# Kernel optimization log

Hardware: AMD Instinct MI355X
Metric: run time of the kernel (lower is better)

Reference implementation:

```python
import jax, jax.numpy as jnp
import numpy as np

D_MODEL = 1024
N_HEAD = 16
HEAD_DIM = D_MODEL // N_HEAD
D_FF = int(D_MODEL * 4.0)
B, T = 2, 2048


def rms_norm(x, eps=1e-6):
    return x * jax.lax.rsqrt(jnp.mean(jnp.square(x), axis=-1, keepdims=True) + eps)


def rope_tables(T, head_dim):
    # half-truncated RoPE: first quarter of dims get real freqs, next quarter zeros
    angular_freq = (1.0 / 1024.0) ** jnp.linspace(0.0, 1.0, head_dim // 4, dtype=jnp.float32)
    angular_freq = jnp.concatenate([angular_freq, jnp.zeros(head_dim // 4, jnp.float32)])
    theta = jnp.arange(T, dtype=jnp.float32)[:, None] * angular_freq[None, :]  # [T, head_dim//2]
    return jnp.cos(theta), jnp.sin(theta)


def apply_rope(x, cos, sin):
    # x: [B, H, T, D]; cos/sin: [T, D//2]
    x1, x2 = jnp.split(x.astype(jnp.float32), 2, axis=-1)
    c = cos[None, None]
    s = sin[None, None]
    y1 = x1 * c + x2 * s
    y2 = -x1 * s + x2 * c
    return jnp.concatenate([y1, y2], axis=-1).astype(x.dtype)


def setup_inputs() -> dict:
    key = jax.random.key(0)
    ks = jax.random.split(key, 10)
    x = jax.random.normal(ks[0], (B, T, D_MODEL), jnp.float32)
    block_mask = jnp.tril(jnp.ones((T, T), jnp.bool_))  # causal
    sc = 1.0 / np.sqrt(D_MODEL)
    Wqkv = jax.random.normal(ks[1], (D_MODEL, 3 * D_MODEL), jnp.float32) * sc
    bqkv = jnp.zeros((3 * D_MODEL,), jnp.float32)
    Wo = jax.random.normal(ks[2], (D_MODEL, D_MODEL), jnp.float32) * sc
    bo = jnp.zeros((D_MODEL,), jnp.float32)
    W1 = jax.random.normal(ks[3], (D_MODEL, D_FF), jnp.float32) * sc
    b1 = jnp.zeros((D_FF,), jnp.float32)
    W2 = jax.random.normal(ks[4], (D_FF, D_MODEL), jnp.float32) * (1.0 / np.sqrt(D_FF))
    b2 = jnp.zeros((D_MODEL,), jnp.float32)
    return {"x": x, "block_mask": block_mask, "Wqkv": Wqkv, "bqkv": bqkv,
            "Wo": Wo, "bo": bo, "W1": W1, "b1": b1, "W2": W2, "b2": b2}


def reference(x, block_mask, Wqkv, bqkv, Wo, bo, W1, b1, W2, b2):
    Bq, Tq, D = x.shape
    cos, sin = rope_tables(Tq, HEAD_DIM)

    def attn(h):
        qkv = h @ Wqkv + bqkv  # [B, T, 3D]
        qkv = qkv.reshape(Bq, Tq, 3, N_HEAD, HEAD_DIM)
        qkv = jnp.transpose(qkv, (2, 0, 3, 1, 4))  # [3, B, H, T, d]
        q, k, v = qkv[0], qkv[1], qkv[2]
        q, k = rms_norm(q), rms_norm(k)
        q, k = apply_rope(q, cos, sin), apply_rope(k, cos, sin)
        scores = jnp.einsum('bhtd,bhsd->bhts', q, k) / np.sqrt(HEAD_DIM)
        scores = jnp.where(block_mask[None, None], scores, jnp.float32(-1e30))
        p = jax.nn.softmax(scores, axis=-1)
        o = jnp.einsum('bhts,bhsd->bhtd', p, v)
        o = jnp.transpose(o, (0, 2, 1, 3)).reshape(Bq, Tq, D)
        return o @ Wo + bo

    def mlp(h):
        return jax.nn.gelu(h @ W1 + b1) @ W2 + b2

    x = x + attn(rms_norm(x))
    x = x + mlp(rms_norm(x))
    return x
```

## Files before the change

### kernel.cpp

```cpp
#include <hip/hip_runtime.h>
#include <hip/hip_bf16.h>


typedef __attribute__((ext_vector_type(8))) short short8;
typedef __attribute__((ext_vector_type(4))) float f32x4;
typedef __attribute__((ext_vector_type(8))) unsigned short u16x8;

#define MROWS 4096
#define DMODEL 1024
#define DFF 4096
#define NH 16
#define HD 64
#define SEQ 2048

static __device__ __forceinline__ unsigned short f2bf(float f) {
    union { __hip_bfloat16 b; unsigned short u; } cv;
    cv.b = __float2bfloat16(f);
    return cv.u;
}

static __device__ __forceinline__ void gload_lds16(const void* g, void* l) {
    __builtin_amdgcn_global_load_lds(
        (const __attribute__((address_space(1))) unsigned int*)g,
        (__attribute__((address_space(3))) unsigned int*)l, 16, 0, 0);
}

static __device__ __forceinline__ int xcd_swizzle(int id, int nwg) {
    const int nx = 8;
    const int q = nwg / nx, r = nwg % nx;
    const int xcd = id % nx, loc = id / nx;
    return (xcd < r ? xcd * (q + 1) : r * (q + 1) + (xcd - r) * q) + loc;
}

__global__ void cast_transpose(const float* __restrict__ W,
                               unsigned short* __restrict__ Wt, int K, int N) {
    __shared__ float tile[32][33];
    const int tx = threadIdx.x & 31;
    const int ty = threadIdx.x >> 5;
    const int n0 = blockIdx.x * 32, k0 = blockIdx.y * 32;
#pragma unroll
    for (int i = 0; i < 4; ++i) {
        int kk = ty + i * 8;
        tile[kk][tx] = W[(long)(k0 + kk) * N + n0 + tx];
    }
    __syncthreads();
#pragma unroll
    for (int i = 0; i < 4; ++i) {
        int nn = ty + i * 8;
        Wt[(long)(n0 + nn) * K + k0 + tx] = f2bf(tile[tx][nn]);
    }
}

__global__ void rope_table(float* __restrict__ cosT, float* __restrict__ sinT) {
    const int t = blockIdx.x, j = threadIdx.x;
    float th = (j < 16) ? (float)t * exp2f(-(10.0f / 15.0f) * (float)j) : 0.0f;
    cosT[t * 32 + j] = cosf(th);
    sinT[t * 32 + j] = sinf(th);
}

__global__ void rmsnorm_cast(const float* __restrict__ xin,
                             unsigned short* __restrict__ hout) {
    const int row = blockIdx.x;
    const float4 v = ((const float4*)(xin + (long)row * DMODEL))[threadIdx.x];
    float ss = v.x * v.x + v.y * v.y + v.z * v.z + v.w * v.w;
#pragma unroll
    for (int m = 32; m >= 1; m >>= 1) ss += __shfl_xor(ss, m);
    __shared__ float part[4];
    if ((threadIdx.x & 63) == 0) part[threadIdx.x >> 6] = ss;
    __syncthreads();
    const float tot = part[0] + part[1] + part[2] + part[3];
    const float sc = rsqrtf(tot * (1.0f / (float)DMODEL) + 1e-6f);
    ushort4 o;
    o.x = f2bf(v.x * sc); o.y = f2bf(v.y * sc);
    o.z = f2bf(v.z * sc); o.w = f2bf(v.w * sc);
    ((ushort4*)hout)[(long)row * (DMODEL / 4) + threadIdx.x] = o;
}

template <int EPI, int BN>
__launch_bounds__(256)
__global__ void gemm_bt(const short* __restrict__ A, const short* __restrict__ Bt,
                        const float* __restrict__ bias, const float* __restrict__ res,
                        float* __restrict__ outF, unsigned short* __restrict__ outB,
                        int N, int K) {
    constexpr int NF = BN / 32;
    __shared__ short As[2][128 * 32];
    __shared__ short Bs[2][BN * 32];
    const int tid = threadIdx.x;
    const int lane = tid & 63, w = tid >> 6;
    const int wr = w >> 1, wc = w & 1;
    const int l16 = lane & 15, lhi = lane >> 4;

    const int nwg = gridDim.x * gridDim.y;
    int id = xcd_swizzle(blockIdx.y * gridDim.x + blockIdx.x, nwg);
    const int bx = id % gridDim.x, by = id / gridDim.x;
    const long rowA0 = (long)by * 128;
    const long rowB0 = (long)bx * BN;

    const f32x4 fz = {0.f, 0.f, 0.f, 0.f};
    f32x4 acc[4][NF];
#pragma unroll
    for (int m = 0; m < 4; ++m)
#pragma unroll
        for (int n = 0; n < NF; ++n) acc[m][n] = fz;

    auto stage = [&](int kt, int b) {
        const int k0 = kt << 5;
#pragma unroll
        for (int it = 0; it < 2; ++it) {
            const int c = it * 256 + tid;
            const int r = c >> 2, col = (c & 3) << 3;
            gload_lds16(A + (rowA0 + r) * K + k0 + col, (char*)As[b] + c * 16);
        }
#pragma unroll
        for (int it = 0; it < BN / 64; ++it) {
            const int c = it * 256 + tid;
            const int r = c >> 2, col = (c & 3) << 3;
            gload_lds16(Bt + (rowB0 + r) * K + k0 + col, (char*)Bs[b] + c * 16);
        }
    };
    auto compute = [&](int b) {
        short8 af[4], bf[NF];
#pragma unroll
        for (int m = 0; m < 4; ++m)
            af[m] = *(const short8*)(&As[b][0] + (wr * 64 + m * 16 + l16) * 32 + lhi * 8);
#pragma unroll
        for (int n = 0; n < NF; ++n)
            bf[n] = *(const short8*)(&Bs[b][0] + (wc * (BN / 2) + n * 16 + l16) * 32 + lhi * 8);
#pragma unroll
        for (int m = 0; m < 4; ++m)
#pragma unroll
            for (int n = 0; n < NF; ++n)
                acc[m][n] = __builtin_amdgcn_mfma_f32_16x16x32_bf16(
                    af[m], bf[n], acc[m][n], 0, 0, 0);
    };

    const int ktiles = K >> 5;
    stage(0, 0);
    __syncthreads();
    int cur = 0;
    for (int kt = 0; kt < ktiles; ++kt) {
        if (kt + 1 < ktiles) stage(kt + 1, cur ^ 1);
        compute(cur);
        __syncthreads();
        cur ^= 1;
    }

#pragma unroll
    for (int m = 0; m < 4; ++m) {
        const long r0 = rowA0 + wr * 64 + m * 16 + lhi * 4;
#pragma unroll
        for (int n = 0; n < NF; ++n) {
            const long cc = rowB0 + wc * (BN / 2) + n * 16 + l16;
            const float bv = bias[cc];
#pragma unroll
            for (int j = 0; j < 4; ++j) {
                const long idx = (r0 + j) * N + cc;
                float v = acc[m][n][j] + bv;
                if (EPI == 1) v += res[idx];
                if (EPI == 2) {
                    float g = 0.5f * v *
                        (1.0f + tanhf(0.7978845608028654f * (v + 0.044715f * v * v * v)));
                    outB[idx] = f2bf(g);
                } else {
                    outF[idx] = v;
                }
            }
        }
    }
}

__global__ void qkv_post(const float* __restrict__ qkv, const float* __restrict__ cosT,
                         const float* __restrict__ sinT, unsigned short* __restrict__ Qo,
                         unsigned short* __restrict__ Ko) {
    const int lane = threadIdx.x & 63;
    const int g = blockIdx.x * 4 + (threadIdx.x >> 6);
    const int row = g >> 4, h = g & 15;
    const int b = row >> 11, t = row & 2047;
    const float* base = qkv + (long)row * 3072 + h * 64;
    float q = base[lane];
    float k = base[1024 + lane];
    float sq = q * q, sk = k * k;
#pragma unroll
    for (int m = 32; m >= 1; m >>= 1) {
        sq += __shfl_xor(sq, m);
        sk += __shfl_xor(sk, m);
    }
    q *= rsqrtf(sq * (1.0f / 64.0f) + 1e-6f);
    k *= rsqrtf(sk * (1.0f / 64.0f) + 1e-6f);
    const int j = lane & 31;
    const float c = cosT[t * 32 + j], s = sinT[t * 32 + j];
    const float q2 = __shfl_xor(q, 32), k2 = __shfl_xor(k, 32);
    const float sgn = (lane < 32) ? 1.0f : -1.0f;
    const float qr = q * c + sgn * q2 * s;
    const float kr = k * c + sgn * k2 * s;
    const long o = ((long)(b * 16 + h) * SEQ + t) * 64 + lane;
    Qo[o] = f2bf(qr * 0.125f);
    Ko[o] = f2bf(kr);
}

__global__ void transpose_v(const float* __restrict__ qkv,
                            unsigned short* __restrict__ Vt) {
    __shared__ float tile[64][65];
    const int tid = threadIdx.x;
    const int bh = blockIdx.x, tt = blockIdx.y;
    const int b = bh >> 4, h = bh & 15;
    const int tr = tid >> 2, c0 = (tid & 3) * 16;
    const float* src = qkv + ((long)(b * SEQ + tt * 64 + tr)) * 3072 + 2048 + h * 64 + c0;
#pragma unroll
    for (int i = 0; i < 4; ++i) {
        float4 v = ((const float4*)src)[i];
        tile[tr][c0 + i * 4 + 0] = v.x;
        tile[tr][c0 + i * 4 + 1] = v.y;
        tile[tr][c0 + i * 4 + 2] = v.z;
        tile[tr][c0 + i * 4 + 3] = v.w;
    }
    __syncthreads();
    const int d = tid >> 2, t0 = (tid & 3) * 16;
    unsigned short* dst = Vt + ((long)bh * 64 + d) * SEQ + tt * 64 + t0;
#pragma unroll
    for (int half = 0; half < 2; ++half) {
        u16x8 o;
#pragma unroll
        for (int e = 0; e < 8; ++e) o[e] = f2bf(tile[t0 + half * 8 + e][d]);
        *(u16x8*)(dst + half * 8) = o;
    }
}

__launch_bounds__(256)
__global__ void attn_fwd(const short* __restrict__ Qg, const short* __restrict__ Kg,
                         const short* __restrict__ Vtg, unsigned short* __restrict__ Og) {
    __shared__ short Ks[64 * 64];
    __shared__ short Vs[64 * 64];
    __shared__ char Ps[4][16 * 128];
    const int tid = threadIdx.x, lane = tid & 63, w = tid >> 6;
    const int l16 = lane & 15, lhi = lane >> 4;
    int id = xcd_swizzle(blockIdx.y * gridDim.x + blockIdx.x, 1024);
    const int bh = id >> 5;
    const int qt = 31 - (id & 31);
    const int bb = bh >> 4, hh = bh & 15;
    const long base_q = (long)bh * (SEQ * 64);

    short8 aq0, aq1;
    {
        const short* Qp = Qg + base_q + (long)(qt * 64 + w * 16) * 64;
        aq0 = *(const short8*)(Qp + l16 * 64 + lhi * 8);
        aq1 = *(const short8*)(Qp + l16 * 64 + 32 + lhi * 8);
    }
    float mrow[4] = {-1e30f, -1e30f, -1e30f, -1e30f};
    float lrow[4] = {0.f, 0.f, 0.f, 0.f};
    const f32x4 fz = {0.f, 0.f, 0.f, 0.f};
    f32x4 oacc[4];
#pragma unroll
    for (int n = 0; n < 4; ++n) oacc[n] = fz;

    char* Pw = &Ps[w][0];

    for (int kt = 0; kt <= qt; ++kt) {
        const short* Kp = Kg + base_q + (long)kt * 64 * 64;
        const short* Vp = Vtg + base_q + (long)kt * 64;
#pragma unroll
        for (int it = 0; it < 2; ++it) {
            const int c = it * 256 + w * 64 + lane;
            const int r = c >> 3;
            const int col = ((c & 7) ^ (r & 7)) << 3;
            gload_lds16(Kp + r * 64 + col, (char*)Ks + c * 16);
            gload_lds16(Vp + (long)r * SEQ + col, (char*)Vs + c * 16);
        }
        __syncthreads();

        f32x4 s[4];
        __builtin_amdgcn_s_setprio(1);
#pragma unroll
        for (int n = 0; n < 4; ++n) {
            const int kr = n * 16 + l16;
            short8 bk0 = *(const short8*)(Ks + kr * 64 + ((lhi ^ (kr & 7)) << 3));
            short8 bk1 = *(const short8*)(Ks + kr * 64 + (((lhi + 4) ^ (kr & 7)) << 3));
            f32x4 z = fz;
            z = __builtin_amdgcn_mfma_f32_16x16x32_bf16(aq0, bk0, z, 0, 0, 0);
            s[n] = __builtin_amdgcn_mfma_f32_16x16x32_bf16(aq1, bk1, z, 0, 0, 0);
        }
        __builtin_amdgcn_s_setprio(0);
        if (kt == qt) {
#pragma unroll
            for (int n = 0; n < 4; ++n)
#pragma unroll
                for (int j = 0; j < 4; ++j)
                    if (n * 16 + l16 > w * 16 + lhi * 4 + j) s[n][j] = -1e30f;
        }

#pragma unroll
        for (int j = 0; j < 4; ++j) {
            float pm = fmaxf(fmaxf(s[0][j], s[1][j]), fmaxf(s[2][j], s[3][j]));
            pm = fmaxf(pm, __shfl_xor(pm, 1));
            pm = fmaxf(pm, __shfl_xor(pm, 2));
            pm = fmaxf(pm, __shfl_xor(pm, 4));
            pm = fmaxf(pm, __shfl_xor(pm, 8));
            const float newm = fmaxf(mrow[j], pm);
            const float sc = __expf(mrow[j] - newm);
            float ps = 0.f;
#pragma unroll
            for (int n = 0; n < 4; ++n) {
                float p = __expf(s[n][j] - newm);
                s[n][j] = p;
                ps += p;
            }
            ps += __shfl_xor(ps, 1);
            ps += __shfl_xor(ps, 2);
            ps += __shfl_xor(ps, 4);
            ps += __shfl_xor(ps, 8);
            lrow[j] = lrow[j] * sc + ps;
            mrow[j] = newm;
#pragma unroll
            for (int n = 0; n < 4; ++n) oacc[n][j] *= sc;
        }

#pragma unroll
        for (int n = 0; n < 4; ++n)
#pragma unroll
            for (int j = 0; j < 4; ++j) {
                const int q = lhi * 4 + j, colp = n * 16 + l16;
                *(short*)(Pw + ((q * 128 + colp * 2) ^ ((q & 7) << 4))) =
                    (short)f2bf(s[n][j]);
            }
        __builtin_amdgcn_s_setprio(1);
#pragma unroll
        for (int ks = 0; ks < 2; ++ks) {
            short8 pa = *(const short8*)(Pw + ((l16 * 128 + ks * 64 + lhi * 16) ^ ((l16 & 7) << 4)));
#pragma unroll
            for (int n = 0; n < 4; ++n) {
                const int dr = n * 16 + l16;
                short8 vb = *(const short8*)(Vs + dr * 64 + ((((ks << 2) + lhi) ^ (dr & 7)) << 3));
                oacc[n] = __builtin_amdgcn_mfma_f32_16x16x32_bf16(pa, vb, oacc[n], 0, 0, 0);
            }
        }
        __builtin_amdgcn_s_setprio(0);
        __syncthreads();
    }

#pragma unroll
    for (int n = 0; n < 4; ++n)
#pragma unroll
        for (int j = 0; j < 4; ++j) {
            const int qrow = qt * 64 + w * 16 + lhi * 4 + j;
            const long orow = (long)bb * SEQ + qrow;
            const int col = hh * 64 + n * 16 + l16;
            Og[orow * DMODEL + col] = f2bf(oacc[n][j] / lrow[j]);
        }
}

extern "C" void kernel_launch(void* const* d_in, const int* in_sizes, int n_in,
                              void* d_out, int out_size, void* d_ws, size_t ws_size,
                              hipStream_t stream) {
    const float* x    = (const float*)d_in[0];
    const float* Wqkv = (const float*)d_in[2];
    const float* bqkv = (const float*)d_in[3];
    const float* Wo   = (const float*)d_in[4];
    const float* bo   = (const float*)d_in[5];
    const float* W1   = (const float*)d_in[6];
    const float* b1   = (const float*)d_in[7];
    const float* W2   = (const float*)d_in[8];
    const float* b2   = (const float*)d_in[9];
    float* out = (float*)d_out;

    char* ws = (char*)d_ws;
    auto alloc = [&](size_t b) {
        char* p = ws;
        ws += (b + 255) & ~(size_t)255;
        return p;
    };
    short* WqkvT = (short*)alloc(3072ull * 1024 * 2);
    short* WoT   = (short*)alloc(1024ull * 1024 * 2);
    short* W1T   = (short*)alloc(4096ull * 1024 * 2);
    short* W2T   = (short*)alloc(1024ull * 4096 * 2);
    float* cosT  = (float*)alloc(2048ull * 32 * 4);
    float* sinT  = (float*)alloc(2048ull * 32 * 4);
    short* hbuf  = (short*)alloc((size_t)MROWS * DMODEL * 2);
    short* Qb    = (short*)alloc(32ull * SEQ * 64 * 2);
    short* Kb    = (short*)alloc(32ull * SEQ * 64 * 2);
    short* Vtb   = (short*)alloc(32ull * 64 * SEQ * 2);
    short* Ob    = (short*)alloc((size_t)MROWS * DMODEL * 2);
    float* x1    = (float*)alloc((size_t)MROWS * DMODEL * 4);
    char*  big   = alloc((size_t)MROWS * 3072 * 4);
    float* qkv   = (float*)big;
    unsigned short* act = (unsigned short*)big;

    cast_transpose<<<dim3(96, 32), 256, 0, stream>>>(Wqkv, (unsigned short*)WqkvT, 1024, 3072);
    cast_transpose<<<dim3(32, 32), 256, 0, stream>>>(Wo, (unsigned short*)WoT, 1024, 1024);
    cast_transpose<<<dim3(128, 32), 256, 0, stream>>>(W1, (unsigned short*)W1T, 1024, 4096);
    cast_transpose<<<dim3(32, 128), 256, 0, stream>>>(W2, (unsigned short*)W2T, 4096, 1024);
    rope_table<<<2048, 32, 0, stream>>>(cosT, sinT);
    rmsnorm_cast<<<MROWS, 256, 0, stream>>>(x, (unsigned short*)hbuf);
    gemm_bt<0, 128><<<dim3(24, 32), 256, 0, stream>>>(hbuf, WqkvT, bqkv, nullptr, qkv, nullptr, 3072, 1024);
    qkv_post<<<16384, 256, 0, stream>>>(qkv, cosT, sinT,
                                        (unsigned short*)Qb, (unsigned short*)Kb);
    transpose_v<<<dim3(32, 32), 256, 0, stream>>>(qkv, (unsigned short*)Vtb);
    attn_fwd<<<dim3(32, 32), 256, 0, stream>>>(Qb, Kb, Vtb, (unsigned short*)Ob);
    gemm_bt<1, 64><<<dim3(16, 32), 256, 0, stream>>>(Ob, WoT, bo, x, x1, nullptr, 1024, 1024);
    rmsnorm_cast<<<MROWS, 256, 0, stream>>>(x1, (unsigned short*)hbuf);
    gemm_bt<2, 128><<<dim3(32, 32), 256, 0, stream>>>(hbuf, W1T, b1, nullptr, nullptr, act, 4096, 1024);
    gemm_bt<1, 64><<<dim3(16, 32), 256, 0, stream>>>((const short*)act, W2T, b2, x1, out, nullptr, 1024, 4096);
}
```

Baseline: 447.8 us.

## Double-buffer K/V in attention, pair causal tiles per block, lazy rescale

The attention kernel now double-buffers the K and V tiles in LDS, prefetching the next key tile while the current one is computed, which removes the load-then-sync stall of each iteration. Each block handles two query tiles (qt and 31-qt) to balance causal work, and the launch grid is halved to match. The S MFMA operands are swapped so each lane holds a full query row, which cuts the per-row shuffle reductions and lets P be written as packed 4-element stores. Online-softmax rescaling is skipped when the running max grows by no more than 8, trading a small overflow-safety margin for fewer exp and multiply operations. Doubling LDS for K/V may reduce occupancy.

```diff
diff --git a/kernel.cpp b/kernel.cpp
--- a/kernel.cpp
+++ b/kernel.cpp
@@ -4,6 +4,7 @@
 
 typedef __attribute__((ext_vector_type(8))) short short8;
 typedef __attribute__((ext_vector_type(4))) float f32x4;
+typedef __attribute__((ext_vector_type(4))) unsigned short u16x4;
 typedef __attribute__((ext_vector_type(8))) unsigned short u16x8;
 
 #define MROWS 4096
@@ -229,123 +230,143 @@
 __launch_bounds__(256)
 __global__ void attn_fwd(const short* __restrict__ Qg, const short* __restrict__ Kg,
                          const short* __restrict__ Vtg, unsigned short* __restrict__ Og) {
-    __shared__ short Ks[64 * 64];
-    __shared__ short Vs[64 * 64];
-    __shared__ char Ps[4][16 * 128];
+    __shared__ short Ks[2][64 * 64];
+    __shared__ short Vs[2][64 * 64];
+    __shared__ char Ps[4][2048];
     const int tid = threadIdx.x, lane = tid & 63, w = tid >> 6;
     const int l16 = lane & 15, lhi = lane >> 4;
-    int id = xcd_swizzle(blockIdx.y * gridDim.x + blockIdx.x, 1024);
-    const int bh = id >> 5;
-    const int qt = 31 - (id & 31);
+    const int id = xcd_swizzle(blockIdx.y * gridDim.x + blockIdx.x, 512);
+    const int bh = id >> 4;
+    const int ip = id & 15;
     const int bb = bh >> 4, hh = bh & 15;
     const long base_q = (long)bh * (SEQ * 64);
-
-    short8 aq0, aq1;
-    {
-        const short* Qp = Qg + base_q + (long)(qt * 64 + w * 16) * 64;
-        aq0 = *(const short8*)(Qp + l16 * 64 + lhi * 8);
-        aq1 = *(const short8*)(Qp + l16 * 64 + 32 + lhi * 8);
-    }
-    float mrow[4] = {-1e30f, -1e30f, -1e30f, -1e30f};
-    float lrow[4] = {0.f, 0.f, 0.f, 0.f};
+    char* Pw = &Ps[w][0];
+    const int swz = (l16 & 7) << 4;
     const f32x4 fz = {0.f, 0.f, 0.f, 0.f};
-    f32x4 oacc[4];
-#pragma unroll
-    for (int n = 0; n < 4; ++n) oacc[n] = fz;
-
-    char* Pw = &Ps[w][0];
-
-    for (int kt = 0; kt <= qt; ++kt) {
-        const short* Kp = Kg + base_q + (long)kt * 64 * 64;
-        const short* Vp = Vtg + base_q + (long)kt * 64;
-#pragma unroll
-        for (int it = 0; it < 2; ++it) {
-            const int c = it * 256 + w * 64 + lane;
-            const int r = c >> 3;
-            const int col = ((c & 7) ^ (r & 7)) << 3;
-            gload_lds16(Kp + r * 64 + col, (char*)Ks + c * 16);
-            gload_lds16(Vp + (long)r * SEQ + col, (char*)Vs + c * 16);
-        }
+
+#pragma unroll 1
+    for (int rep = 0; rep < 2; ++rep) {
+        const int qt = rep ? ip : 31 - ip;
+        short8 aq0, aq1;
+        {
+            const short* Qp = Qg + base_q + (long)(qt * 64 + w * 16) * 64;
+            aq0 = *(const short8*)(Qp + l16 * 64 + lhi * 8);
+            aq1 = *(const short8*)(Qp + l16 * 64 + 32 + lhi * 8);
+        }
+        float mrow = -1e30f, lrow = 0.f;
+        f32x4 oacc[4];
+#pragma unroll
+        for (int n = 0; n < 4; ++n) oacc[n] = fz;
+
+        auto stage = [&](int kt, int b) {
+            const short* Kp = Kg + base_q + (long)kt * 64 * 64;
+            const short* Vp = Vtg + base_q + (long)kt * 64;
+#pragma unroll
+            for (int it = 0; it < 2; ++it) {
+                const int c = it * 256 + tid;
+                const int r = c >> 3;
+                const int col = ((c & 7) ^ (r & 7)) << 3;
+                gload_lds16(Kp + r * 64 + col, (char*)&Ks[b][0] + c * 16);
+                gload_lds16(Vp + (long)r * SEQ + col, (char*)&Vs[b][0] + c * 16);
+            }
+        };
+
+        stage(0, 0);
         __syncthreads();
-
-        f32x4 s[4];
-        __builtin_amdgcn_s_setprio(1);
-#pragma unroll
-        for (int n = 0; n < 4; ++n) {
-            const int kr = n * 16 + l16;
-            short8 bk0 = *(const short8*)(Ks + kr * 64 + ((lhi ^ (kr & 7)) << 3));
-            short8 bk1 = *(const short8*)(Ks + kr * 64 + (((lhi + 4) ^ (kr & 7)) << 3));
-            f32x4 z = fz;
-            z = __builtin_amdgcn_mfma_f32_16x16x32_bf16(aq0, bk0, z, 0, 0, 0);
-            s[n] = __builtin_amdgcn_mfma_f32_16x16x32_bf16(aq1, bk1, z, 0, 0, 0);
-        }
-        __builtin_amdgcn_s_setprio(0);
-        if (kt == qt) {
+        int cur = 0;
+        for (int kt = 0; kt <= qt; ++kt) {
+            if (kt < qt) stage(kt + 1, cur ^ 1);
+            const short* KsC = &Ks[cur][0];
+            const short* VsC = &Vs[cur][0];
+
+            f32x4 s[4];
+            __builtin_amdgcn_s_setprio(1);
+#pragma unroll
+            for (int n = 0; n < 4; ++n) {
+                const int kr = n * 16 + l16;
+                short8 bk0 = *(const short8*)(KsC + kr * 64 + ((lhi ^ (kr & 7)) << 3));
+                short8 bk1 = *(const short8*)(KsC + kr * 64 + (((lhi + 4) ^ (kr & 7)) << 3));
+                f32x4 z = fz;
+                z = __builtin_amdgcn_mfma_f32_16x16x32_bf16(bk0, aq0, z, 0, 0, 0);
+                s[n] = __builtin_amdgcn_mfma_f32_16x16x32_bf16(bk1, aq1, z, 0, 0, 0);
+            }
+            __builtin_amdgcn_s_setprio(0);
+            if (kt == qt) {
+#pragma unroll
+                for (int n = 0; n < 4; ++n)
+#pragma unroll
+                    for (int j = 0; j < 4; ++j)
+                        if (n * 16 + lhi * 4 + j > w * 16 + l16) s[n][j] = -1e30f;
+            }
+
+            float pm = s[0][0];
 #pragma unroll
             for (int n = 0; n < 4; ++n)
 #pragma unroll
-                for (int j = 0; j < 4; ++j)
-                    if (n * 16 + l16 > w * 16 + lhi * 4 + j) s[n][j] = -1e30f;
+                for (int j = 0; j < 4; ++j) pm = fmaxf(pm, s[n][j]);
+            pm = fmaxf(pm, __shfl_xor(pm, 16));
+            pm = fmaxf(pm, __shfl_xor(pm, 32));
+            if (!__all(pm <= mrow + 8.f)) {
+                const float newm = fmaxf(mrow, pm);
+                const float sc = __expf(mrow - newm);
+                mrow = newm;
+                lrow *= sc;
+#pragma unroll
+                for (int j = 0; j < 4; ++j) {
+                    const float scj = __shfl(sc, lhi * 4 + j);
+#pragma unroll
+                    for (int n = 0; n < 4; ++n) oacc[n][j] *= scj;
+                }
+            }
+            float ps = 0.f;
+#pragma unroll
+            for (int n = 0; n < 4; ++n)
+#pragma unroll
+                for (int j = 0; j < 4; ++j) {
+                    const float p = __expf(s[n][j] - mrow);
+                    s[n][j] = p;
+                    ps += p;
+                }
+            ps += __shfl_xor(ps, 16);
+            ps += __shfl_xor(ps, 32);
+            lrow += ps;
+
+#pragma unroll
+            for (int n = 0; n < 4; ++n) {
+                u16x4 pk;
+                pk[0] = f2bf(s[n][0]);
+                pk[1] = f2bf(s[n][1]);
+                pk[2] = f2bf(s[n][2]);
+                pk[3] = f2bf(s[n][3]);
+                *(u16x4*)(Pw + ((l16 * 128 + n * 32 + lhi * 8) ^ swz)) = pk;
+            }
+
+            __builtin_amdgcn_s_setprio(1);
+#pragma unroll
+            for (int ks = 0; ks < 2; ++ks) {
+                short8 pa = *(const short8*)(Pw + ((l16 * 128 + ks * 64 + lhi * 16) ^ swz));
+#pragma unroll
+                for (int n = 0; n < 4; ++n) {
+                    const int dr = n * 16 + l16;
+                    short8 vb = *(const short8*)(VsC + dr * 64 + ((((ks << 2) + lhi) ^ (dr & 7)) << 3));
+                    oacc[n] = __builtin_amdgcn_mfma_f32_16x16x32_bf16(pa, vb, oacc[n], 0, 0, 0);
+                }
+            }
+            __builtin_amdgcn_s_setprio(0);
+            __syncthreads();
+            cur ^= 1;
         }
 
 #pragma unroll
         for (int j = 0; j < 4; ++j) {
-            float pm = fmaxf(fmaxf(s[0][j], s[1][j]), fmaxf(s[2][j], s[3][j]));
-            pm = fmaxf(pm, __shfl_xor(pm, 1));
-            pm = fmaxf(pm, __shfl_xor(pm, 2));
-            pm = fmaxf(pm, __shfl_xor(pm, 4));
-            pm = fmaxf(pm, __shfl_xor(pm, 8));
-            const float newm = fmaxf(mrow[j], pm);
-            const float sc = __expf(mrow[j] - newm);
-            float ps = 0.f;
-#pragma unroll
-            for (int n = 0; n < 4; ++n) {
-                float p = __expf(s[n][j] - newm);
-                s[n][j] = p;
-                ps += p;
-            }
-            ps += __shfl_xor(ps, 1);
-            ps += __shfl_xor(ps, 2);
-            ps += __shfl_xor(ps, 4);
-            ps += __shfl_xor(ps, 8);
-            lrow[j] = lrow[j] * sc + ps;
-            mrow[j] = newm;
-#pragma unroll
-            for (int n = 0; n < 4; ++n) oacc[n][j] *= sc;
-        }
-
-#pragma unroll
-        for (int n = 0; n < 4; ++n)
-#pragma unroll
-            for (int j = 0; j < 4; ++j) {
-                const int q = lhi * 4 + j, colp = n * 16 + l16;
-                *(short*)(Pw + ((q * 128 + colp * 2) ^ ((q & 7) << 4))) =
-                    (short)f2bf(s[n][j]);
-            }
-        __builtin_amdgcn_s_setprio(1);
-#pragma unroll
-        for (int ks = 0; ks < 2; ++ks) {
-            short8 pa = *(const short8*)(Pw + ((l16 * 128 + ks * 64 + lhi * 16) ^ ((l16 & 7) << 4)));
-#pragma unroll
-            for (int n = 0; n < 4; ++n) {
-                const int dr = n * 16 + l16;
-                short8 vb = *(const short8*)(Vs + dr * 64 + ((((ks << 2) + lhi) ^ (dr & 7)) << 3));
-                oacc[n] = __builtin_amdgcn_mfma_f32_16x16x32_bf16(pa, vb, oacc[n], 0, 0, 0);
-            }
-        }
-        __builtin_amdgcn_s_setprio(0);
-        __syncthreads();
-    }
-
-#pragma unroll
-    for (int n = 0; n < 4; ++n)
-#pragma unroll
-        for (int j = 0; j < 4; ++j) {
+            const float lr = __shfl(lrow, lhi * 4 + j);
             const int qrow = qt * 64 + w * 16 + lhi * 4 + j;
             const long orow = (long)bb * SEQ + qrow;
-            const int col = hh * 64 + n * 16 + l16;
-            Og[orow * DMODEL + col] = f2bf(oacc[n][j] / lrow[j]);
-        }
+#pragma unroll
+            for (int n = 0; n < 4; ++n)
+                Og[orow * DMODEL + hh * 64 + n * 16 + l16] = f2bf(oacc[n][j] / lr);
+        }
+    }
 }
 
 extern "C" void kernel_launch(void* const* d_in, const int* in_sizes, int n_in,
@@ -394,7 +415,7 @@
     qkv_post<<<16384, 256, 0, stream>>>(qkv, cosT, sinT,
                                         (unsigned short*)Qb, (unsigned short*)Kb);
     transpose_v<<<dim3(32, 32), 256, 0, stream>>>(qkv, (unsigned short*)Vtb);
-    attn_fwd<<<dim3(32, 32), 256, 0, stream>>>(Qb, Kb, Vtb, (unsigned short*)Ob);
+    attn_fwd<<<dim3(16, 32), 256, 0, stream>>>(Qb, Kb, Vtb, (unsigned short*)Ob);
     gemm_bt<1, 64><<<dim3(16, 32), 256, 0, stream>>>(Ob, WoT, bo, x, x1, nullptr, 1024, 1024);
     rmsnorm_cast<<<MROWS, 256, 0, stream>>>(x1, (unsigned short*)hbuf);
     gemm_bt<2, 128><<<dim3(32, 32), 256, 0, stream>>>(hbuf, W1T, b1, nullptr, nullptr, act, 4096, 1024);
```

New measurement: 402.5 us. 1.11x faster.
